# Optimization experiments

Hardware: AMD Instinct MI355X
Metric: run time of the kernel (lower is better)

The kernel has to match this reference:

```python
import jax, jax.numpy as jnp
import numpy as np

N, COLS, K, OUT = 200000, 784, 10, 2

def setup_inputs() -> dict:
    key = jax.random.key(0)
    ks = jax.random.split(key, 7)
    def lin_init(k, fan_in, fan_out):
        # torch Linear default: U(-1/sqrt(fan_in), 1/sqrt(fan_in))
        bound = 1.0 / np.sqrt(fan_in)
        return jax.random.uniform(k, (fan_in, fan_out), jnp.float32, -bound, bound)
    return {
        "data": jax.random.normal(ks[0], (N, COLS), jnp.float32),
        "idxs": jax.random.randint(ks[1], (N, K), 0, N),
        "W1": lin_init(ks[2], COLS, 128), "b1": jnp.zeros((128,), jnp.float32),
        "W2": lin_init(ks[3], 128, 64),  "b2": jnp.zeros((64,), jnp.float32),
        "W3": lin_init(ks[4], 64, 32),   "b3": jnp.zeros((32,), jnp.float32),
        "Wout": lin_init(ks[5], 32, OUT), "bout": jnp.zeros((OUT,), jnp.float32),
    }

def reference(data, idxs, W1, b1, W2, b2, W3, b3, Wout, bout):
    # MLP: (Linear + ReLU) x 3, then final Linear (no activation)
    h = jax.nn.relu(data @ W1 + b1)
    h = jax.nn.relu(h @ W2 + b2)
    h = jax.nn.relu(h @ W3 + b3)
    projected = h @ Wout + bout                      # [N, OUT]
    nb = projected[idxs]                             # [N, K, OUT] gather
    d = jnp.sum((projected[:, None, :] - nb) ** 2, axis=-1)  # [N, K]
    return d.reshape(-1, 1)                          # [N*K, 1]
```

## Files before the change

kernel.cpp:

```cpp
#include <hip/hip_runtime.h>
#include <stdint.h>

typedef float f32x4 __attribute__((ext_vector_type(4)));

__global__ __launch_bounds__(256) void mlp_kernel(
    const float* __restrict__ data,
    const float* __restrict__ W1, const float* __restrict__ b1,
    const float* __restrict__ W2, const float* __restrict__ b2,
    const float* __restrict__ W3, const float* __restrict__ b3,
    const float* __restrict__ Wout, const float* __restrict__ bout,
    float* __restrict__ proj)
{
    __shared__ __align__(16) char smem[51200];
    float* a_s  = (float*)(smem);
    float* w1_s = (float*)(smem + 17408);
    float* h1s  = (float*)(smem);
    float* w2s  = (float*)(smem + 33792);
    float* h2s  = (float*)(smem);
    float* w3s  = (float*)(smem + 17408);

    const int tid = threadIdx.x;
    const size_t row0 = (size_t)blockIdx.x * 64;

    const int srow = tid >> 2, sq = tid & 3;
    const int rg = tid >> 4,  cg = tid & 15;

    float acc[4][8];
    #pragma unroll
    for (int r = 0; r < 4; ++r)
        #pragma unroll
        for (int j = 0; j < 8; ++j) acc[r][j] = 0.f;

    for (int it = 0; it < 13; ++it) {
        const int kbase = it * 64;
        #pragma unroll
        for (int j = 0; j < 4; ++j) {
            int col = kbase + sq*16 + j*4;
            f32x4 v = (f32x4){0.f, 0.f, 0.f, 0.f};
            if (col < 784) v = *(const f32x4*)(data + (row0 + srow)*784 + col);
            *(f32x4*)(a_s + srow*68 + sq*16 + j*4) = v;
        }
        {
            const int gk = kbase + srow;
            #pragma unroll
            for (int j = 0; j < 8; ++j) {
                f32x4 v = (f32x4){0.f, 0.f, 0.f, 0.f};
                if (gk < 784) v = *(const f32x4*)(W1 + (size_t)gk*128 + sq*32 + j*4);
                *(f32x4*)(w1_s + srow*132 + sq*32 + j*4) = v;
            }
        }
        __syncthreads();
        #pragma unroll 4
        for (int kk = 0; kk < 64; ++kk) {
            f32x4 w0 = *(const f32x4*)(w1_s + kk*132 + cg*8);
            f32x4 w1v = *(const f32x4*)(w1_s + kk*132 + cg*8 + 4);
            #pragma unroll
            for (int r = 0; r < 4; ++r) {
                float a = a_s[(rg*4 + r)*68 + kk];
                #pragma unroll
                for (int c = 0; c < 4; ++c) {
                    acc[r][c]     += a * w0[c];
                    acc[r][4 + c] += a * w1v[c];
                }
            }
        }
        __syncthreads();
    }
    #pragma unroll
    for (int r = 0; r < 4; ++r) {
        const int m = rg*4 + r;
        #pragma unroll
        for (int j = 0; j < 8; ++j) {
            const int col = cg*8 + j;
            float v = acc[r][j] + b1[col];
            h1s[m*132 + col] = v > 0.f ? v : 0.f;
        }
    }
    #pragma unroll
    for (int j = 0; j < 4; ++j) {
        int wi = j*1024 + tid*4;
        *(f32x4*)(w2s + wi) = *(const f32x4*)(W2 + wi);
    }
    __syncthreads();

    const int m2 = tid >> 2, nq = tid & 3;
    float h2a[16];
    #pragma unroll
    for (int i = 0; i < 16; ++i) h2a[i] = b2[nq*16 + i];
    #pragma unroll
    for (int p = 0; p < 2; ++p) {
        if (p == 1) {
            __syncthreads();
            #pragma unroll
            for (int j = 0; j < 4; ++j) {
                int wi = j*1024 + tid*4;
                *(f32x4*)(w2s + wi) = *(const f32x4*)(W2 + 4096 + wi);
            }
            __syncthreads();
        }
        for (int q = 0; q < 16; ++q) {
            f32x4 hq = *(const f32x4*)(h1s + m2*132 + p*64 + q*4);
            #pragma unroll
            for (int kk = 0; kk < 4; ++kk) {
                #pragma unroll
                for (int i = 0; i < 4; ++i) {
                    f32x4 wv = *(const f32x4*)(w2s + (q*4 + kk)*64 + nq*16 + i*4);
                    #pragma unroll
                    for (int c = 0; c < 4; ++c) h2a[i*4 + c] += hq[kk] * wv[c];
                }
            }
        }
    }
    __syncthreads();
    #pragma unroll
    for (int i = 0; i < 4; ++i) {
        f32x4 v;
        #pragma unroll
        for (int c = 0; c < 4; ++c) { float x = h2a[i*4 + c]; v[c] = x > 0.f ? x : 0.f; }
        *(f32x4*)(h2s + m2*68 + nq*16 + i*4) = v;
    }
    #pragma unroll
    for (int j = 0; j < 2; ++j) {
        int wi = j*1024 + tid*4;
        *(f32x4*)(w3s + wi) = *(const f32x4*)(W3 + wi);
    }
    __syncthreads();

    const int m3 = tid >> 2, nq3 = tid & 3;
    float h3a[8];
    #pragma unroll
    for (int i = 0; i < 8; ++i) h3a[i] = b3[nq3*8 + i];
    for (int q = 0; q < 16; ++q) {
        f32x4 hq = *(const f32x4*)(h2s + m3*68 + q*4);
        #pragma unroll
        for (int kk = 0; kk < 4; ++kk) {
            #pragma unroll
            for (int i2 = 0; i2 < 2; ++i2) {
                f32x4 wv = *(const f32x4*)(w3s + (q*4 + kk)*32 + nq3*8 + i2*4);
                #pragma unroll
                for (int c = 0; c < 4; ++c) h3a[i2*4 + c] += hq[kk] * wv[c];
            }
        }
    }
    float p0 = 0.f, p1 = 0.f;
    #pragma unroll
    for (int i = 0; i < 8; ++i) {
        const int k = nq3*8 + i;
        float h = h3a[i] > 0.f ? h3a[i] : 0.f;
        p0 += h * Wout[k*2 + 0];
        p1 += h * Wout[k*2 + 1];
    }
    p0 += __shfl_xor(p0, 1); p0 += __shfl_xor(p0, 2);
    p1 += __shfl_xor(p1, 1); p1 += __shfl_xor(p1, 2);
    if (nq3 == 0) {
        proj[(row0 + m3)*2 + 0] = p0 + bout[0];
        proj[(row0 + m3)*2 + 1] = p1 + bout[1];
    }
}

__global__ __launch_bounds__(256) void dist_kernel(
    const float* __restrict__ proj, const int* __restrict__ idxs,
    float* __restrict__ out, int total)
{
    int gid = blockIdx.x * 256 + threadIdx.x;
    if (gid >= total) return;
    unsigned i = (unsigned)gid / 10u;
    unsigned j = (unsigned)idxs[gid];
    float dx = proj[i*2 + 0] - proj[j*2 + 0];
    float dy = proj[i*2 + 1] - proj[j*2 + 1];
    out[gid] = dx*dx + dy*dy;
}

extern "C" void kernel_launch(void* const* d_in, const int* in_sizes, int n_in,
                              void* d_out, int out_size, void* d_ws, size_t ws_size,
                              hipStream_t stream)
{
    const float* data = (const float*)d_in[0];
    const int*   idxs = (const int*)d_in[1];
    const float* W1   = (const float*)d_in[2];
    const float* b1   = (const float*)d_in[3];
    const float* W2   = (const float*)d_in[4];
    const float* b2   = (const float*)d_in[5];
    const float* W3   = (const float*)d_in[6];
    const float* b3   = (const float*)d_in[7];
    const float* Wout = (const float*)d_in[8];
    const float* bout = (const float*)d_in[9];

    const int N = in_sizes[0] / 784;
    float* proj = (float*)d_ws;

    mlp_kernel<<<N / 64, 256, 0, stream>>>(data, W1, b1, W2, b2, W3, b3, Wout, bout, proj);
    dist_kernel<<<(N*10 + 255) / 256, 256, 0, stream>>>(proj, idxs, (float*)d_out, N*10);
}
```

Measured before the change: 714.1 us.

## Shrink LDS tiles, swizzle A tile, and stream W2 in small chunks

The layer-1 K tile is halved from 64 to 32 and the activation tile is stored with an XOR swizzle, so each thread can read float4 vectors of A instead of scalars. W2 is now streamed through LDS in eight 4 KB chunks rather than two 16 KB halves. Together these cut the LDS footprint to about 37 KB, and launch_bounds now requests four blocks per CU to raise occupancy. The cost is twice as many K iterations and barriers in layer 1, more barriers in layer 2, and possible register spilling under the tighter register limit.

New measurement: 691.3 us. 1.03x faster.

```diff
diff --git a/kernel.cpp b/kernel.cpp
--- a/kernel.cpp
+++ b/kernel.cpp
@@ -3,7 +3,7 @@
 
 typedef float f32x4 __attribute__((ext_vector_type(4)));
 
-__global__ __launch_bounds__(256) void mlp_kernel(
+__global__ __launch_bounds__(256, 4) void mlp_kernel(
     const float* __restrict__ data,
     const float* __restrict__ W1, const float* __restrict__ b1,
     const float* __restrict__ W2, const float* __restrict__ b2,
@@ -11,9 +11,9 @@
     const float* __restrict__ Wout, const float* __restrict__ bout,
     float* __restrict__ proj)
 {
-    __shared__ __align__(16) char smem[51200];
+    __shared__ __align__(16) char smem[37888];
     float* a_s  = (float*)(smem);
-    float* w1_s = (float*)(smem + 17408);
+    float* w1_s = (float*)(smem + 8192);
     float* h1s  = (float*)(smem);
     float* w2s  = (float*)(smem + 33792);
     float* h2s  = (float*)(smem);
@@ -22,45 +22,58 @@
     const int tid = threadIdx.x;
     const size_t row0 = (size_t)blockIdx.x * 64;
 
-    const int srow = tid >> 2, sq = tid & 3;
-    const int rg = tid >> 4,  cg = tid & 15;
+    const int ty = tid & 15;
+    const int tx = tid >> 4;
 
     float acc[4][8];
     #pragma unroll
     for (int r = 0; r < 4; ++r)
         #pragma unroll
-        for (int j = 0; j < 8; ++j) acc[r][j] = 0.f;
+        for (int c = 0; c < 8; ++c) acc[r][c] = 0.f;
 
-    for (int it = 0; it < 13; ++it) {
-        const int kbase = it * 64;
-        #pragma unroll
-        for (int j = 0; j < 4; ++j) {
-            int col = kbase + sq*16 + j*4;
-            f32x4 v = (f32x4){0.f, 0.f, 0.f, 0.f};
-            if (col < 784) v = *(const f32x4*)(data + (row0 + srow)*784 + col);
-            *(f32x4*)(a_s + srow*68 + sq*16 + j*4) = v;
+    for (int it = 0; it < 25; ++it) {
+        const int kbase = it * 32;
+        {
+            const int sr = tid >> 2, q = tid & 3;
+            #pragma unroll
+            for (int j = 0; j < 2; ++j) {
+                const int kg = q + 4*j;
+                const int col = kbase + kg*4;
+                f32x4 v = (f32x4){0.f, 0.f, 0.f, 0.f};
+                if (col < 784) v = *(const f32x4*)(data + (row0 + sr)*784 + col);
+                *(f32x4*)(a_s + sr*32 + ((kg ^ ((sr >> 2) & 7)) << 2)) = v;
+            }
         }
         {
-            const int gk = kbase + srow;
+            const int kr = tid >> 3, c8 = tid & 7;
+            const int gk = kbase + kr;
             #pragma unroll
-            for (int j = 0; j < 8; ++j) {
+            for (int j = 0; j < 4; ++j) {
+                const int col = c8*4 + 32*j;
                 f32x4 v = (f32x4){0.f, 0.f, 0.f, 0.f};
-                if (gk < 784) v = *(const f32x4*)(W1 + (size_t)gk*128 + sq*32 + j*4);
-                *(f32x4*)(w1_s + srow*132 + sq*32 + j*4) = v;
+                if (gk < 784) v = *(const f32x4*)(W1 + (size_t)gk*128 + col);
+                *(f32x4*)(w1_s + kr*132 + col) = v;
             }
         }
         __syncthreads();
-        #pragma unroll 4
-        for (int kk = 0; kk < 64; ++kk) {
-            f32x4 w0 = *(const f32x4*)(w1_s + kk*132 + cg*8);
-            f32x4 w1v = *(const f32x4*)(w1_s + kk*132 + cg*8 + 4);
+        #pragma unroll
+        for (int kt = 0; kt < 8; ++kt) {
+            f32x4 av[4];
             #pragma unroll
-            for (int r = 0; r < 4; ++r) {
-                float a = a_s[(rg*4 + r)*68 + kk];
+            for (int r = 0; r < 4; ++r)
+                av[r] = *(const f32x4*)(a_s + (ty*4 + r)*32 + ((kt ^ (ty & 7)) << 2));
+            #pragma unroll
+            for (int kk = 0; kk < 4; ++kk) {
+                f32x4 w0  = *(const f32x4*)(w1_s + (kt*4 + kk)*132 + tx*8);
+                f32x4 w1v = *(const f32x4*)(w1_s + (kt*4 + kk)*132 + tx*8 + 4);
                 #pragma unroll
-                for (int c = 0; c < 4; ++c) {
-                    acc[r][c]     += a * w0[c];
-                    acc[r][4 + c] += a * w1v[c];
+                for (int r = 0; r < 4; ++r) {
+                    const float a = av[r][kk];
+                    #pragma unroll
+                    for (int c = 0; c < 4; ++c) {
+                        acc[r][c]     += a * w0[c];
+                        acc[r][4 + c] += a * w1v[c];
+                    }
                 }
             }
         }
@@ -68,38 +81,26 @@
     }
     #pragma unroll
     for (int r = 0; r < 4; ++r) {
-        const int m = rg*4 + r;
+        const int m = ty*4 + r;
         #pragma unroll
-        for (int j = 0; j < 8; ++j) {
-            const int col = cg*8 + j;
-            float v = acc[r][j] + b1[col];
+        for (int c = 0; c < 8; ++c) {
+            const int col = tx*8 + c;
+            float v = acc[r][c] + b1[col];
             h1s[m*132 + col] = v > 0.f ? v : 0.f;
         }
     }
-    #pragma unroll
-    for (int j = 0; j < 4; ++j) {
-        int wi = j*1024 + tid*4;
-        *(f32x4*)(w2s + wi) = *(const f32x4*)(W2 + wi);
-    }
-    __syncthreads();
 
     const int m2 = tid >> 2, nq = tid & 3;
     float h2a[16];
     #pragma unroll
     for (int i = 0; i < 16; ++i) h2a[i] = b2[nq*16 + i];
-    #pragma unroll
-    for (int p = 0; p < 2; ++p) {
-        if (p == 1) {
-            __syncthreads();
-            #pragma unroll
-            for (int j = 0; j < 4; ++j) {
-                int wi = j*1024 + tid*4;
-                *(f32x4*)(w2s + wi) = *(const f32x4*)(W2 + 4096 + wi);
-            }
-            __syncthreads();
-        }
-        for (int q = 0; q < 16; ++q) {
-            f32x4 hq = *(const f32x4*)(h1s + m2*132 + p*64 + q*4);
+    for (int p = 0; p < 8; ++p) {
+        if (p) __syncthreads();
+        *(f32x4*)(w2s + tid*4) = *(const f32x4*)(W2 + p*1024 + tid*4);
+        __syncthreads();
+        #pragma unroll
+        for (int q = 0; q < 4; ++q) {
+            f32x4 hq = *(const f32x4*)(h1s + m2*132 + p*16 + q*4);
             #pragma unroll
             for (int kk = 0; kk < 4; ++kk) {
                 #pragma unroll
```
